# Kernel optimization log

Hardware: AMD Instinct MI355X
Metric: run time of the kernel (lower is better)

Reference implementation:

```python
import jax, jax.numpy as jnp
import numpy as np

B, S, D, H = 4, 2048, 256, 4
DH = D // H  # per-head dim (shared for q, k, v)


def setup_inputs() -> dict:
    key = jax.random.key(0)
    ks = jax.random.split(key, 10)
    scale = 1.0 / np.sqrt(D)
    return {
        "q": jax.random.normal(ks[0], (B, S, D), jnp.float32),
        "k": jax.random.normal(ks[1], (B, S, D), jnp.float32),
        "v": jax.random.normal(ks[2], (B, S, D), jnp.float32),
        "mask": jax.random.randint(ks[3], (B, S, S), 0, 2).astype(bool),
        # per-head query/key projections: [H, D, DH] (+ bias [H, DH])
        "Wq": jax.random.uniform(ks[4], (H, D, DH), jnp.float32, -scale, scale),
        "bq": jax.random.uniform(ks[5], (H, DH), jnp.float32, -scale, scale),
        "Wk": jax.random.uniform(ks[6], (H, D, DH), jnp.float32, -scale, scale),
        "bk": jax.random.uniform(ks[7], (H, DH), jnp.float32, -scale, scale),
        # shared value projection: [D, DH]
        "Wv": jax.random.uniform(ks[8], (D, DH), jnp.float32, -scale, scale),
        "bv": jnp.zeros((DH,), jnp.float32),
        # final projection (no bias): [DH, D]
        "Wf": jax.random.uniform(ks[9], (DH, D), jnp.float32, -scale, scale),
    }


def reference(q, k, v, mask, Wq, bq, Wk, bk, Wv, bv, Wf):
    # per-head projections (all heads at once): [B, H, S, DH]
    q_h = jnp.einsum("bsd,hde->bhse", q, Wq) + bq[None, :, None, :]
    k_h = jnp.einsum("bsd,hde->bhse", k, Wk) + bk[None, :, None, :]
    # shared value projection: [B, S, DH]
    v_p = v @ Wv + bv
    # scaled scores: [B, H, S, S]
    scores = jnp.einsum("bhse,bhte->bhst", q_h, k_h) / jnp.sqrt(
        jnp.asarray(DH, q_h.dtype)
    )
    scores = jnp.where(mask[:, None, :, :], jnp.asarray(-1e9, scores.dtype), scores)
    attn = jax.nn.softmax(scores, axis=-1)  # [B, H, S, S]
    # shared V for every head: [B, H, S, DH]
    heads = jnp.einsum("bhst,bte->bhse", attn, v_p)
    mean_head = heads.mean(axis=1)  # [B, S, DH]
    out = mean_head @ Wf  # [B, S, D]
    return out, attn
```

## Files before the change

### kernel.cpp

```cpp
#include <hip/hip_runtime.h>
#include <stdint.h>
#include <stddef.h>

#define B_ 4
#define S_ 2048
#define D_ 256
#define H_ 4
#define DH_ 64
#define NTT 64
#define SC_LOG2E 0.18033688011112042f

typedef __attribute__((ext_vector_type(8))) short short8;
typedef __attribute__((ext_vector_type(4))) short short4v;
typedef __attribute__((ext_vector_type(4))) float f32x4;
typedef unsigned int uint;

__device__ __forceinline__ short bf16_rne(float f) {
  union { float f; uint32_t u; } c; c.f = f;
  uint32_t u = c.u + 0x7FFFu + ((c.u >> 16) & 1u);
  return (short)(u >> 16);
}

__device__ __forceinline__ f32x4 mfma16(short8 a, short8 b, f32x4 c) {
  return __builtin_amdgcn_mfma_f32_16x16x32_bf16(a, b, c, 0, 0, 0);
}

__device__ __forceinline__ void gl_lds16(const short* g, short* l) {
  __builtin_amdgcn_global_load_lds(
      (const __attribute__((address_space(1))) unsigned int*)g,
      (__attribute__((address_space(3))) unsigned int*)l, 16, 0, 0);
}

__global__ void prep_weights(const float* __restrict__ Wq, const float* __restrict__ Wk,
                             const float* __restrict__ Wv,
                             short* __restrict__ WqT, short* __restrict__ WkT,
                             short* __restrict__ WvT) {
  int tid = blockIdx.x * blockDim.x + threadIdx.x;
  if (tid < 65536) {
    int n = tid >> 8, d = tid & 255;
    int hh = n >> 6, e = n & 63;
    WqT[tid] = bf16_rne(Wq[((size_t)hh * D_ + d) * DH_ + e] * SC_LOG2E);
    WkT[tid] = bf16_rne(Wk[((size_t)hh * D_ + d) * DH_ + e]);
  } else if (tid < 65536 + 16384) {
    int t2 = tid - 65536;
    int e = t2 >> 8, d = t2 & 255;
    WvT[t2] = bf16_rne(Wv[(size_t)d * DH_ + e]);
  }
}

__global__ void detect_kernel(const unsigned int* __restrict__ m, int* __restrict__ flag) {
  __shared__ int isbool;
  if (threadIdx.x == 0) isbool = 0;
  __syncthreads();
#pragma unroll
  for (int i = 0; i < 4; ++i) {
    unsigned int d = m[threadIdx.x + i * 256];
    if (d & 0xFFFFFFFEu) isbool = 1;
  }
  __syncthreads();
  if (threadIdx.x == 0) *flag = isbool ? 0 : 1;
}

__global__ __launch_bounds__(256) void pack_mask(const unsigned char* __restrict__ maskB,
                                                 const int* __restrict__ flagp,
                                                 uint* __restrict__ mbits) {
  int tid = blockIdx.x * 256 + threadIdx.x;
  uint w = 0;
  if (*flagp) {
    const uint4* p = (const uint4*)((const uint*)maskB + (size_t)tid * 32);
#pragma unroll
    for (int i = 0; i < 8; ++i) {
      uint4 d = p[i];
      w |= (d.x ? 1u : 0u) << (i * 4);
      w |= (d.y ? 1u : 0u) << (i * 4 + 1);
      w |= (d.z ? 1u : 0u) << (i * 4 + 2);
      w |= (d.w ? 1u : 0u) << (i * 4 + 3);
    }
  } else {
    const uint4* p = (const uint4*)(maskB + (size_t)tid * 32);
#pragma unroll
    for (int i = 0; i < 2; ++i) {
      uint4 d = p[i];
      const uint* dw = (const uint*)&d;
#pragma unroll
      for (int j = 0; j < 4; ++j) {
        uint x = dw[j];
        int base = i * 16 + j * 4;
        w |= ((x & 0x000000FFu) ? 1u : 0u) << (base);
        w |= ((x & 0x0000FF00u) ? 1u : 0u) << (base + 1);
        w |= ((x & 0x00FF0000u) ? 1u : 0u) << (base + 2);
        w |= ((x & 0xFF000000u) ? 1u : 0u) << (base + 3);
      }
    }
  }
  mbits[tid] = w;
}

__global__ __launch_bounds__(256) void proj_kernel(
    const float* __restrict__ X, const short* __restrict__ WT,
    const float* __restrict__ bias, short* __restrict__ outp, int vmode, float bscale) {
  const int b = blockIdx.z;
  const int s0 = blockIdx.x * 64;
  const int n0 = blockIdx.y * 64;
  const int tid = threadIdx.x;
  const int wave = tid >> 6, lane = tid & 63;
  const int lr = lane & 15, lg = lane >> 4;

  const int arowi = s0 + wave * 16 + lr;
  const float* xr = X + ((size_t)b * S_ + arowi) * D_;

  f32x4 zero4 = {0.f, 0.f, 0.f, 0.f};
  f32x4 acc[4];
#pragma unroll
  for (int ct = 0; ct < 4; ++ct) acc[ct] = zero4;

#pragma unroll
  for (int c = 0; c < 8; ++c) {
    const int k0 = c * 32 + lg * 8;
    f32x4 x0 = *(const f32x4*)(xr + k0);
    f32x4 x1 = *(const f32x4*)(xr + k0 + 4);
    short8 a;
#pragma unroll
    for (int jj = 0; jj < 4; ++jj) { a[jj] = bf16_rne(x0[jj]); a[4 + jj] = bf16_rne(x1[jj]); }
#pragma unroll
    for (int ct = 0; ct < 4; ++ct) {
      short8 bw = *(const short8*)(WT + (size_t)(n0 + ct * 16 + lr) * D_ + k0);
      acc[ct] = mfma16(a, bw, acc[ct]);
    }
  }

  if (vmode == 0) {
#pragma unroll
    for (int ct = 0; ct < 4; ++ct) {
      int n = n0 + ct * 16 + lr;
      float bb = bias[n] * bscale;
      int hh = n >> 6, e = n & 63;
#pragma unroll
      for (int r = 0; r < 4; ++r) {
        int srow = s0 + wave * 16 + lg * 4 + r;
        outp[(((size_t)b * H_ + hh) * S_ + srow) * DH_ + e] = bf16_rne(acc[ct][r] + bb);
      }
    }
  } else {
#pragma unroll
    for (int ct = 0; ct < 4; ++ct) {
      int n = n0 + ct * 16 + lr;
      float bb = bias[n];
      int s4 = s0 + wave * 16 + lg * 4;
      short4v pk;
#pragma unroll
      for (int r = 0; r < 4; ++r) pk[r] = bf16_rne(acc[ct][r] + bb);
      *(short4v*)(outp + ((size_t)b * DH_ + n) * S_ + s4) = pk;
    }
  }
}

__device__ __forceinline__ void stageK64(const short* Ksrc, short* dst, int wq, int lane) {
#pragma unroll
  for (int i = 0; i < 2; ++i) {
    int ub = i * 256 + wq * 64;
    int u = ub + lane;
    int row = u >> 3, c = (u ^ row) & 7;
    gl_lds16(Ksrc + (size_t)row * 64 + c * 8, dst + (size_t)ub * 8);
  }
}

__device__ __forceinline__ void stageV64(const short* Vb, int t0, short* dst, int wq, int lane) {
#pragma unroll
  for (int i = 0; i < 2; ++i) {
    int ub = i * 256 + wq * 64;
    int u = ub + lane;
    int er = u >> 3, c = (u ^ er) & 7;
    gl_lds16(Vb + (size_t)er * S_ + t0 + c * 8, dst + (size_t)ub * 8);
  }
}

__global__ __launch_bounds__(512, 4) void attn_kernel(
    const short* __restrict__ qh, const short* __restrict__ kh,
    const short* __restrict__ vT, const uint* __restrict__ mbits,
    float* __restrict__ attn, float* __restrict__ heads) {
  __shared__ __align__(16) short Kt[2][2][4096];
  __shared__ __align__(16) short Vt[2][2][4096];
  __shared__ __align__(16) short Pt[8][1024];

  const int flat = blockIdx.x;
  const int xcd = flat & 7;
  const int pos = flat >> 3;
  const int bh_i = xcd * 2 + (pos >> 5);
  const int q0 = (pos & 31) * 64;
  const int b = bh_i >> 2, h = bh_i & 3;

  const int tid = threadIdx.x;
  const int wave = tid >> 6, lane = tid & 63;
  const int half = wave >> 2, wq = wave & 3;
  const int lr = lane & 15, lg = lane >> 4;
  const int tbase = half * (S_ / 2);

  const size_t bh = (size_t)b * H_ + h;
  const short* Qb = qh + bh * S_ * DH_;
  const short* Kb = kh + bh * S_ * DH_;
  const short* Vb = vT + (size_t)b * DH_ * S_;

  const int qrow = q0 + wq * 16 + lr;
  const uint* mrow = mbits + ((size_t)b * S_ + qrow) * (S_ / 32);
  float* arow = attn + (bh * S_ + qrow) * S_;

  const short8 aq0 = *(const short8*)(Qb + (size_t)qrow * DH_ + lg * 8);
  const short8 aq1 = *(const short8*)(Qb + (size_t)qrow * DH_ + 32 + lg * 8);

  short* pw = &Pt[wave][0];

  float rsum = 0.f;
  stageK64(Kb + (size_t)tbase * DH_, Kt[half][0], wq, lane);
  asm volatile("s_waitcnt vmcnt(0)" ::: "memory");
  __builtin_amdgcn_s_barrier();
  int cur = 0;
  for (int tt = 0; tt < 16; ++tt) {
    const int t0 = tbase + tt * NTT;
    uint2 mv = *(const uint2*)(mrow + (t0 >> 5));
    if (tt + 1 < 16) {
      stageK64(Kb + (size_t)(t0 + NTT) * DH_, Kt[half][cur ^ 1], wq, lane);
      asm volatile("s_waitcnt vmcnt(3)" ::: "memory");
    } else {
      asm volatile("s_waitcnt vmcnt(1)" ::: "memory");
    }
    __builtin_amdgcn_s_barrier();
    const short* kt = Kt[half][cur];
#pragma unroll
    for (int j = 0; j < 4; ++j) {
      int row = j * 16 + lr;
      short8 bk0 = *(const short8*)(kt + row * 64 + (((lg) ^ row) & 7) * 8);
      short8 bk1 = *(const short8*)(kt + row * 64 + (((lg + 4) ^ row) & 7) * 8);
      f32x4 acc = {0.f, 0.f, 0.f, 0.f};
      acc = mfma16(bk0, aq0, acc);
      acc = mfma16(bk1, aq1, acc);
      uint mw = (j < 2) ? mv.x : mv.y;
#pragma unroll
      for (int r = 0; r < 4; ++r) {
        int sh = (j & 1) * 16 + lg * 4 + r;
        float p = ((mw >> sh) & 1u) ? 0.f : __builtin_exp2f(acc[r]);
        rsum += p;
      }
    }
    __builtin_amdgcn_s_barrier();
    cur ^= 1;
  }
  rsum += __shfl_xor(rsum, 16);
  rsum += __shfl_xor(rsum, 32);
  float* fsum = (float*)&Pt[0][0];
  if (lane < 16) fsum[wave * 16 + lr] = rsum;
  __syncthreads();
  const float rinv = 1.0f / (fsum[wq * 16 + lr] + fsum[(wq + 4) * 16 + lr]);

  f32x4 o[4];
#pragma unroll
  for (int ct = 0; ct < 4; ++ct) o[ct] = (f32x4){0.f, 0.f, 0.f, 0.f};

  stageK64(Kb + (size_t)tbase * DH_, Kt[half][0], wq, lane);
  stageV64(Vb, tbase, Vt[half][0], wq, lane);
  asm volatile("s_waitcnt vmcnt(0)" ::: "memory");
  __syncthreads();
  cur = 0;
  for (int tt = 0; tt < 16; ++tt) {
    const int t0 = tbase + tt * NTT;
    uint2 mv = *(const uint2*)(mrow + (t0 >> 5));
    if (tt + 1 < 16) {
      stageK64(Kb + (size_t)(t0 + NTT) * DH_, Kt[half][cur ^ 1], wq, lane);
      stageV64(Vb, t0 + NTT, Vt[half][cur ^ 1], wq, lane);
      asm volatile("s_waitcnt vmcnt(9)" ::: "memory");
    } else {
      asm volatile("s_waitcnt vmcnt(5)" ::: "memory");
    }
    __builtin_amdgcn_s_barrier();
    const short* kt = Kt[half][cur];
    const short* vt = Vt[half][cur];
#pragma unroll
    for (int j = 0; j < 4; ++j) {
      int row = j * 16 + lr;
      short8 bk0 = *(const short8*)(kt + row * 64 + (((lg) ^ row) & 7) * 8);
      short8 bk1 = *(const short8*)(kt + row * 64 + (((lg + 4) ^ row) & 7) * 8);
      f32x4 acc = {0.f, 0.f, 0.f, 0.f};
      acc = mfma16(bk0, aq0, acc);
      acc = mfma16(bk1, aq1, acc);
      uint mw = (j < 2) ? mv.x : mv.y;
      f32x4 pst;
      short4v pk;
#pragma unroll
      for (int r = 0; r < 4; ++r) {
        int sh = (j & 1) * 16 + lg * 4 + r;
        float p = ((mw >> sh) & 1u) ? 0.f : __builtin_exp2f(acc[r]) * rinv;
        pst[r] = p;
        pk[r] = bf16_rne(p);
      }
      *(f32x4*)(arow + t0 + j * 16 + lg * 4) = pst;
      *(short4v*)(pw + lr * 64 + (((2 * j + (lg >> 1)) ^ lr) & 7) * 8 + (lg & 1) * 4) = pk;
    }
    short8 apf[2];
#pragma unroll
    for (int kc = 0; kc < 2; ++kc)
      apf[kc] = *(const short8*)(pw + lr * 64 + (((4 * kc + lg) ^ lr) & 7) * 8);
#pragma unroll
    for (int ct = 0; ct < 4; ++ct) {
      int er = ct * 16 + lr;
#pragma unroll
      for (int kc = 0; kc < 2; ++kc) {
        short8 bvf = *(const short8*)(vt + er * 64 + (((4 * kc + lg) ^ er) & 7) * 8);
        o[ct] = mfma16(bvf, apf[kc], o[ct]);
      }
    }
    __builtin_amdgcn_s_barrier();
    cur ^= 1;
  }

  float* ocomb = (float*)&Pt[0][0];
  if (half == 1) {
#pragma unroll
    for (int ct = 0; ct < 4; ++ct)
      *(f32x4*)(ocomb + wq * 1024 + lr * 64 + ct * 16 + lg * 4) = o[ct];
  }
  __syncthreads();
  if (half == 0) {
#pragma unroll
    for (int ct = 0; ct < 4; ++ct) {
      f32x4 t = *(const f32x4*)(ocomb + wq * 1024 + lr * 64 + ct * 16 + lg * 4);
      f32x4 s = o[ct];
      s[0] += t[0]; s[1] += t[1]; s[2] += t[2]; s[3] += t[3];
      *(f32x4*)(heads + (bh * S_ + qrow) * DH_ + ct * 16 + lg * 4) = s;
    }
  }
}

__global__ __launch_bounds__(256) void final_kernel(
    const float* __restrict__ heads, const float* __restrict__ Wf,
    float* __restrict__ outp) {
  __shared__ float mean[16][DH_];
  const int row0 = blockIdx.x * 16;
  const int tid = threadIdx.x;
#pragma unroll
  for (int i = 0; i < 4; ++i) {
    int idx = tid + i * 256;
    int r = idx >> 6, e = idx & 63;
    int gs = row0 + r;
    int bb = gs >> 11, ss = gs & (S_ - 1);
    float acc = 0.f;
#pragma unroll
    for (int hh = 0; hh < H_; ++hh)
      acc += heads[(((size_t)bb * H_ + hh) * S_ + ss) * DH_ + e];
    mean[r][e] = acc * 0.25f;
  }
  __syncthreads();
  float acc[16];
#pragma unroll
  for (int r = 0; r < 16; ++r) acc[r] = 0.f;
  for (int e = 0; e < DH_; ++e) {
    float wf = Wf[(size_t)e * D_ + tid];
#pragma unroll
    for (int r = 0; r < 16; ++r) acc[r] += mean[r][e] * wf;
  }
#pragma unroll
  for (int r = 0; r < 16; ++r)
    outp[(size_t)(row0 + r) * D_ + tid] = acc[r];
}

extern "C" void kernel_launch(void* const* d_in, const int* in_sizes, int n_in,
                              void* d_out, int out_size, void* d_ws, size_t ws_size,
                              hipStream_t stream) {
  (void)in_sizes; (void)n_in; (void)out_size; (void)ws_size;
  const float* q  = (const float*)d_in[0];
  const float* k  = (const float*)d_in[1];
  const float* v  = (const float*)d_in[2];
  const unsigned char* mask = (const unsigned char*)d_in[3];
  const float* Wq = (const float*)d_in[4];
  const float* bq = (const float*)d_in[5];
  const float* Wk = (const float*)d_in[6];
  const float* bk = (const float*)d_in[7];
  const float* Wv = (const float*)d_in[8];
  const float* bv = (const float*)d_in[9];
  const float* Wf = (const float*)d_in[10];

  float* out  = (float*)d_out;
  float* attn = out + (size_t)B_ * S_ * D_;

  char* ws = (char*)d_ws;
  short* qh    = (short*)(ws);
  short* kh    = (short*)(ws + 4194304);
  short* vT    = (short*)(ws + 8388608);
  short* WqT   = (short*)(ws + 9437184);
  short* WkT   = (short*)(ws + 9568256);
  short* WvT   = (short*)(ws + 9699328);
  float* heads = (float*)(ws + 9732096);
  int*   flag  = (int*)(ws + 18120704);
  uint*  mbits = (uint*)(ws + 18120768);

  detect_kernel<<<1, 256, 0, stream>>>((const unsigned int*)mask, flag);
  pack_mask<<<2048, 256, 0, stream>>>(mask, flag, mbits);
  prep_weights<<<320, 256, 0, stream>>>(Wq, Wk, Wv, WqT, WkT, WvT);
  proj_kernel<<<dim3(32, 4, B_), 256, 0, stream>>>(q, WqT, bq, qh, 0, SC_LOG2E);
  proj_kernel<<<dim3(32, 4, B_), 256, 0, stream>>>(k, WkT, bk, kh, 0, 1.0f);
  proj_kernel<<<dim3(32, 1, B_), 256, 0, stream>>>(v, WvT, bv, vT, 1, 1.0f);
  attn_kernel<<<512, 512, 0, stream>>>(qh, kh, vT, mbits, attn, heads);
  final_kernel<<<512, 256, 0, stream>>>(heads, Wf, out);
}
```

Measured before the change: 174.1 us.

## Cache bf16 exp scores in registers to skip recomputing QK^T in pass two

The first pass now stores unnormalized exp(scores) packed as bf16 in a 16x8 register array. The second pass reuses these values, scaled by the row reciprocal sum, instead of restaging K and redoing the QK^T MFMAs and exponentials. This also drops the mask reads in pass two, and V staging begins during the sum reduction. The cost is about 128 extra VGPRs per thread: launch bounds drop from 4 to 2 blocks per CU, and the fp32 attention output is now computed from bf16-rounded probabilities, so it loses precision.

```diff
diff --git a/kernel.cpp b/kernel.cpp
--- a/kernel.cpp
+++ b/kernel.cpp
@@ -175,7 +175,7 @@
   }
 }
 
-__global__ __launch_bounds__(512, 4) void attn_kernel(
+__global__ __launch_bounds__(512, 2) void attn_kernel(
     const short* __restrict__ qh, const short* __restrict__ kh,
     const short* __restrict__ vT, const uint* __restrict__ mbits,
     float* __restrict__ attn, float* __restrict__ heads) {
@@ -210,22 +210,24 @@
 
   short* pw = &Pt[wave][0];
 
+  uint pcache[16][8];
+
   float rsum = 0.f;
   stageK64(Kb + (size_t)tbase * DH_, Kt[half][0], wq, lane);
   asm volatile("s_waitcnt vmcnt(0)" ::: "memory");
   __builtin_amdgcn_s_barrier();
-  int cur = 0;
+#pragma unroll
   for (int tt = 0; tt < 16; ++tt) {
     const int t0 = tbase + tt * NTT;
     uint2 mv = *(const uint2*)(mrow + (t0 >> 5));
     if (tt + 1 < 16) {
-      stageK64(Kb + (size_t)(t0 + NTT) * DH_, Kt[half][cur ^ 1], wq, lane);
+      stageK64(Kb + (size_t)(t0 + NTT) * DH_, Kt[half][(tt + 1) & 1], wq, lane);
       asm volatile("s_waitcnt vmcnt(3)" ::: "memory");
     } else {
-      asm volatile("s_waitcnt vmcnt(1)" ::: "memory");
+      asm volatile("s_waitcnt vmcnt(0)" ::: "memory");
     }
     __builtin_amdgcn_s_barrier();
-    const short* kt = Kt[half][cur];
+    const short* kt = Kt[half][tt & 1];
 #pragma unroll
     for (int j = 0; j < 4; ++j) {
       int row = j * 16 + lr;
@@ -235,65 +237,59 @@
       acc = mfma16(bk0, aq0, acc);
       acc = mfma16(bk1, aq1, acc);
       uint mw = (j < 2) ? mv.x : mv.y;
+      float p[4];
 #pragma unroll
       for (int r = 0; r < 4; ++r) {
         int sh = (j & 1) * 16 + lg * 4 + r;
-        float p = ((mw >> sh) & 1u) ? 0.f : __builtin_exp2f(acc[r]);
-        rsum += p;
+        p[r] = ((mw >> sh) & 1u) ? 0.f : __builtin_exp2f(acc[r]);
+        rsum += p[r];
       }
+      asm("v_cvt_pk_bf16_f32 %0, %1, %2" : "=v"(pcache[tt][j * 2])     : "v"(p[0]), "v"(p[1]));
+      asm("v_cvt_pk_bf16_f32 %0, %1, %2" : "=v"(pcache[tt][j * 2 + 1]) : "v"(p[2]), "v"(p[3]));
     }
     __builtin_amdgcn_s_barrier();
-    cur ^= 1;
   }
   rsum += __shfl_xor(rsum, 16);
   rsum += __shfl_xor(rsum, 32);
+
+  stageV64(Vb, tbase, Vt[half][0], wq, lane);
+
   float* fsum = (float*)&Pt[0][0];
   if (lane < 16) fsum[wave * 16 + lr] = rsum;
   __syncthreads();
   const float rinv = 1.0f / (fsum[wq * 16 + lr] + fsum[(wq + 4) * 16 + lr]);
+  asm volatile("s_waitcnt vmcnt(0)" ::: "memory");
+  __syncthreads();
 
   f32x4 o[4];
 #pragma unroll
   for (int ct = 0; ct < 4; ++ct) o[ct] = (f32x4){0.f, 0.f, 0.f, 0.f};
 
-  stageK64(Kb + (size_t)tbase * DH_, Kt[half][0], wq, lane);
-  stageV64(Vb, tbase, Vt[half][0], wq, lane);
-  asm volatile("s_waitcnt vmcnt(0)" ::: "memory");
-  __syncthreads();
-  cur = 0;
+#pragma unroll
   for (int tt = 0; tt < 16; ++tt) {
     const int t0 = tbase + tt * NTT;
-    uint2 mv = *(const uint2*)(mrow + (t0 >> 5));
     if (tt + 1 < 16) {
-      stageK64(Kb + (size_t)(t0 + NTT) * DH_, Kt[half][cur ^ 1], wq, lane);
-      stageV64(Vb, t0 + NTT, Vt[half][cur ^ 1], wq, lane);
-      asm volatile("s_waitcnt vmcnt(9)" ::: "memory");
+      stageV64(Vb, t0 + NTT, Vt[half][(tt + 1) & 1], wq, lane);
+      asm volatile("s_waitcnt vmcnt(6)" ::: "memory");
     } else {
-      asm volatile("s_waitcnt vmcnt(5)" ::: "memory");
+      asm volatile("s_waitcnt vmcnt(4)" ::: "memory");
     }
     __builtin_amdgcn_s_barrier();
-    const short* kt = Kt[half][cur];
-    const short* vt = Vt[half][cur];
+    const short* vt = Vt[half][tt & 1];
 #pragma unroll
     for (int j = 0; j < 4; ++j) {
-      int row = j * 16 + lr;
-      short8 bk0 = *(const short8*)(kt + row * 64 + (((lg) ^ row) & 7) * 8);
-      short8 bk1 = *(const short8*)(kt + row * 64 + (((lg + 4) ^ row) & 7) * 8);
-      f32x4 acc = {0.f, 0.f, 0.f, 0.f};
-      acc = mfma16(bk0, aq0, acc);
-      acc = mfma16(bk1, aq1, acc);
-      uint mw = (j < 2) ? mv.x : mv.y;
-      f32x4 pst;
-      short4v pk;
-#pragma unroll
-      for (int r = 0; r < 4; ++r) {
-        int sh = (j & 1) * 16 + lg * 4 + r;
-        float p = ((mw >> sh) & 1u) ? 0.f : __builtin_exp2f(acc[r]) * rinv;
-        pst[r] = p;
-        pk[r] = bf16_rne(p);
-      }
+      uint d0 = pcache[tt][j * 2], d1 = pcache[tt][j * 2 + 1];
+      float p0 = __uint_as_float(d0 << 16) * rinv;
+      float p1 = __uint_as_float(d0 & 0xFFFF0000u) * rinv;
+      float p2 = __uint_as_float(d1 << 16) * rinv;
+      float p3 = __uint_as_float(d1 & 0xFFFF0000u) * rinv;
+      f32x4 pst = {p0, p1, p2, p3};
       *(f32x4*)(arow + t0 + j * 16 + lg * 4) = pst;
-      *(short4v*)(pw + lr * 64 + (((2 * j + (lg >> 1)) ^ lr) & 7) * 8 + (lg & 1) * 4) = pk;
+      uint b0, b1;
+      asm("v_cvt_pk_bf16_f32 %0, %1, %2" : "=v"(b0) : "v"(p0), "v"(p1));
+      asm("v_cvt_pk_bf16_f32 %0, %1, %2" : "=v"(b1) : "v"(p2), "v"(p3));
+      uint2 pkd; pkd.x = b0; pkd.y = b1;
+      *(uint2*)(pw + lr * 64 + (((2 * j + (lg >> 1)) ^ lr) & 7) * 8 + (lg & 1) * 4) = pkd;
     }
     short8 apf[2];
 #pragma unroll
@@ -309,7 +305,6 @@
       }
     }
     __builtin_amdgcn_s_barrier();
-    cur ^= 1;
   }
 
   float* ocomb = (float*)&Pt[0][0];
```

Result: slower. 180.8 us (+3.8%).
